# Kernel optimization log

Hardware: AMD Instinct MI355X
Metric: run time of the kernel (lower is better)

The kernel has to match this reference:

```python
import jax, jax.numpy as jnp
import numpy as np

B, D, T_TEXT, T_MEL = 32, 384, 512, 4096


def _make_onehot_path(key, b, t_text, t_mel):
    # Monotonic alignment: for each mel frame, a (sorted) text-token index,
    # then one-hot encode -> [b, t_text, t_mel] binary path matrix.
    idx = jax.random.randint(key, (b, t_mel), 0, t_text)  # [B, T_mel]
    idx = jnp.sort(idx, axis=-1)                           # monotonic in time
    # one-hot over the text axis -> [B, T_mel, T_text] -> transpose
    path = jax.nn.one_hot(idx, t_text, dtype=jnp.float32)  # [B, T_mel, T_text]
    return jnp.transpose(path, (0, 2, 1))                  # [B, T_text, T_mel]


def setup_inputs() -> dict:
    key = jax.random.key(0)
    kx, kp = jax.random.split(key)
    x = jax.random.normal(kx, (B, D, T_TEXT), dtype=jnp.float32)
    path = _make_onehot_path(kp, B, T_TEXT, T_MEL)
    return {"x": x, "path": path}


def reference(x, path):
    # LengthRegulator.forward: x @ path
    # x: [B, D, T_text], path: [B, T_text, T_mel] -> [B, D, T_mel]
    return jnp.einsum("bdn,bnm->bdm", x, path)
```

## Files before the change

### kernel.cpp

```cpp
#include <hip/hip_runtime.h>


#define BATCH   32
#define DIM     384
#define T_TEXT  512
#define T_MEL   4096
#define ROWS    8

typedef float  nfloat4 __attribute__((ext_vector_type(4)));

__global__ __launch_bounds__(256) void find_idx_kernel(
    const float* __restrict__ path,
    int*   __restrict__ idx_ws,
    float* __restrict__ scale_ws)
{
    const int b = blockIdx.y;
    const int m = blockIdx.x * 256 + threadIdx.x;
    const float* pcol = path + (size_t)b * T_TEXT * T_MEL + m;

    int start = (m & ~63) / 8 - 24;
    if (start < 0) start = 0;

    int   idx   = 0;
    float scale = 0.0f;
    bool  found = false;

    for (int n = start; n < T_TEXT; n += 16) {
        float v[16];
        #pragma unroll
        for (int j = 0; j < 16; ++j) {
            const int row = n + j;
            v[j] = (row < T_TEXT) ? pcol[(size_t)row * T_MEL] : 0.0f;
        }
        #pragma unroll
        for (int j = 0; j < 16; ++j)
            if (v[j] != 0.0f) { idx = n + j; scale = v[j]; found = true; }
        if (__all(found)) break;
    }
    if (!__all(found)) {
        for (int n = 0; n < T_TEXT; n += 16) {
            float v[16];
            #pragma unroll
            for (int j = 0; j < 16; ++j) {
                const int row = n + j;
                v[j] = (row < T_TEXT) ? pcol[(size_t)row * T_MEL] : 0.0f;
            }
            #pragma unroll
            for (int j = 0; j < 16; ++j)
                if (!found && v[j] != 0.0f) { idx = n + j; scale = v[j]; found = true; }
            if (__all(found)) break;
        }
    }
    idx_ws[b * T_MEL + m]   = idx;
    scale_ws[b * T_MEL + m] = scale;
}

__global__ __launch_bounds__(256) void gather_kernel(
    const float* __restrict__ x,
    const int*   __restrict__ idx_ws,
    const float* __restrict__ scale_ws,
    float* __restrict__ out)
{
    const int dg = blockIdx.x;
    const int b  = blockIdx.y;
    const int t  = threadIdx.x;

    __shared__ float xs[ROWS * T_TEXT];
    const float* xr = x + ((size_t)b * DIM + dg * ROWS) * T_TEXT;
    #pragma unroll
    for (int i = 0; i < ROWS * T_TEXT / 1024; ++i) {
        const int off = i * 1024 + t * 4;
        *(nfloat4*)(xs + off) = *(const nfloat4*)(xr + off);
    }

    const int*   ip = idx_ws   + b * T_MEL;
    const float* sp = scale_ws + b * T_MEL;
    int4   i4[4];
    float4 s4[4];
    #pragma unroll
    for (int mt = 0; mt < 4; ++mt) {
        const int m4 = mt * 1024 + t * 4;
        i4[mt] = *(const int4*)  (ip + m4);
        s4[mt] = *(const float4*)(sp + m4);
    }
    __syncthreads();

    float* orow = out + ((size_t)b * DIM + dg * ROWS) * T_MEL;
    #pragma unroll
    for (int r = 0; r < ROWS; ++r) {
        const float* xsr = xs + r * T_TEXT;
        #pragma unroll
        for (int mt = 0; mt < 4; ++mt) {
            const int m4 = mt * 1024 + t * 4;
            nfloat4 o;
            o.x = xsr[i4[mt].x] * s4[mt].x;
            o.y = xsr[i4[mt].y] * s4[mt].y;
            o.z = xsr[i4[mt].z] * s4[mt].z;
            o.w = xsr[i4[mt].w] * s4[mt].w;
            __builtin_nontemporal_store(o, (nfloat4*)(orow + (size_t)r * T_MEL + m4));
        }
    }
}

extern "C" void kernel_launch(void* const* d_in, const int* in_sizes, int n_in,
                              void* d_out, int out_size, void* d_ws, size_t ws_size,
                              hipStream_t stream) {
    (void)in_sizes; (void)n_in; (void)ws_size; (void)out_size;
    const float* x    = (const float*)d_in[0];
    const float* path = (const float*)d_in[1];
    float*       out  = (float*)d_out;

    int*   idx_ws   = (int*)d_ws;
    float* scale_ws = (float*)((char*)d_ws + (size_t)BATCH * T_MEL * sizeof(int));

    dim3 g1(T_MEL / 256, BATCH);
    find_idx_kernel<<<g1, dim3(256), 0, stream>>>(path, idx_ws, scale_ws);

    dim3 g2(DIM / ROWS, BATCH);
    gather_kernel<<<g2, dim3(256), 0, stream>>>(x, idx_ws, scale_ws, out);
}
```

Measured before the change: 380.2 us.

## Use fixed-width window search for path index and shrink gather row tile

The index-finding kernel now loads a fixed 48-row window around the expected diagonal position in one unrolled batch, instead of looping in 16-row chunks with wave-wide early exit, and falls back to a full scan only if that misses. The gather kernel drops from 8 to 2 rows per block, which gives more, smaller blocks with one vector load each to stage x, and it switches nontemporal stores to normal stores. The window relies on the sorted random alignment staying near the diagonal, which holds for these inputs, though the fallback keeps it correct in general. The smaller tile reloads the idx and scale arrays more often, in exchange for more parallelism.

```diff
diff --git a/kernel.cpp b/kernel.cpp
--- a/kernel.cpp
+++ b/kernel.cpp
@@ -5,9 +5,10 @@
 #define DIM     384
 #define T_TEXT  512
 #define T_MEL   4096
-#define ROWS    8
+#define WIN     48
+#define ROWS    2
 
-typedef float  nfloat4 __attribute__((ext_vector_type(4)));
+typedef float nfloat4 __attribute__((ext_vector_type(4)));
 
 __global__ __launch_bounds__(256) void find_idx_kernel(
     const float* __restrict__ path,
@@ -18,36 +19,30 @@
     const int m = blockIdx.x * 256 + threadIdx.x;
     const float* pcol = path + (size_t)b * T_TEXT * T_MEL + m;
 
-    int start = (m & ~63) / 8 - 24;
+    int start = ((m & ~63) >> 3) - 20;
     if (start < 0) start = 0;
+    if (start > T_TEXT - WIN) start = T_TEXT - WIN;
 
     int   idx   = 0;
     float scale = 0.0f;
     bool  found = false;
 
-    for (int n = start; n < T_TEXT; n += 16) {
-        float v[16];
-        #pragma unroll
-        for (int j = 0; j < 16; ++j) {
-            const int row = n + j;
-            v[j] = (row < T_TEXT) ? pcol[(size_t)row * T_MEL] : 0.0f;
-        }
-        #pragma unroll
-        for (int j = 0; j < 16; ++j)
-            if (v[j] != 0.0f) { idx = n + j; scale = v[j]; found = true; }
-        if (__all(found)) break;
-    }
+    float v[WIN];
+    #pragma unroll
+    for (int j = 0; j < WIN; ++j)
+        v[j] = pcol[(size_t)(start + j) * T_MEL];
+    #pragma unroll
+    for (int j = 0; j < WIN; ++j)
+        if (v[j] != 0.0f) { idx = start + j; scale = v[j]; found = true; }
+
     if (!__all(found)) {
         for (int n = 0; n < T_TEXT; n += 16) {
-            float v[16];
+            float u[16];
             #pragma unroll
-            for (int j = 0; j < 16; ++j) {
-                const int row = n + j;
-                v[j] = (row < T_TEXT) ? pcol[(size_t)row * T_MEL] : 0.0f;
-            }
+            for (int j = 0; j < 16; ++j) u[j] = pcol[(size_t)(n + j) * T_MEL];
             #pragma unroll
             for (int j = 0; j < 16; ++j)
-                if (!found && v[j] != 0.0f) { idx = n + j; scale = v[j]; found = true; }
+                if (!found && u[j] != 0.0f) { idx = n + j; scale = u[j]; found = true; }
             if (__all(found)) break;
         }
     }
@@ -66,38 +61,36 @@
     const int t  = threadIdx.x;
 
     __shared__ float xs[ROWS * T_TEXT];
+
     const float* xr = x + ((size_t)b * DIM + dg * ROWS) * T_TEXT;
-    #pragma unroll
-    for (int i = 0; i < ROWS * T_TEXT / 1024; ++i) {
-        const int off = i * 1024 + t * 4;
-        *(nfloat4*)(xs + off) = *(const nfloat4*)(xr + off);
-    }
+    const nfloat4 xstage = *(const nfloat4*)(xr + t * 4);
 
     const int*   ip = idx_ws   + b * T_MEL;
     const float* sp = scale_ws + b * T_MEL;
     int4   i4[4];
     float4 s4[4];
     #pragma unroll
-    for (int mt = 0; mt < 4; ++mt) {
-        const int m4 = mt * 1024 + t * 4;
-        i4[mt] = *(const int4*)  (ip + m4);
-        s4[mt] = *(const float4*)(sp + m4);
+    for (int s = 0; s < 4; ++s) {
+        const int m4 = s * 1024 + t * 4;
+        i4[s] = *(const int4*)  (ip + m4);
+        s4[s] = *(const float4*)(sp + m4);
     }
+    *(nfloat4*)(xs + t * 4) = xstage;
     __syncthreads();
 
-    float* orow = out + ((size_t)b * DIM + dg * ROWS) * T_MEL;
+    float* ob = out + ((size_t)b * DIM + dg * ROWS) * T_MEL;
     #pragma unroll
     for (int r = 0; r < ROWS; ++r) {
         const float* xsr = xs + r * T_TEXT;
         #pragma unroll
-        for (int mt = 0; mt < 4; ++mt) {
-            const int m4 = mt * 1024 + t * 4;
+        for (int s = 0; s < 4; ++s) {
+            const int m4 = s * 1024 + t * 4;
             nfloat4 o;
-            o.x = xsr[i4[mt].x] * s4[mt].x;
-            o.y = xsr[i4[mt].y] * s4[mt].y;
-            o.z = xsr[i4[mt].z] * s4[mt].z;
-            o.w = xsr[i4[mt].w] * s4[mt].w;
-            __builtin_nontemporal_store(o, (nfloat4*)(orow + (size_t)r * T_MEL + m4));
+            o.x = xsr[i4[s].x] * s4[s].x;
+            o.y = xsr[i4[s].y] * s4[s].y;
+            o.z = xsr[i4[s].z] * s4[s].z;
+            o.w = xsr[i4[s].w] * s4[s].w;
+            *(nfloat4*)(ob + (size_t)r * T_MEL + m4) = o;
         }
     }
 }
```

New measurement: 386.6 us. Within noise of the previous version (+1.7%).
